# Kernel optimization log

Hardware: AMD Instinct MI355X
Metric: run time of the kernel (lower is better)

The kernel has to match this reference:

```python
import jax, jax.numpy as jnp
import numpy as np

B, W, D, R = 8, 1024, 1024, 64
GAMMA_MIN, GAMMA_MAX, ALPHA_CAP, EPS = 0.15, 1.0, 1.0, 1e-8


def _linear_init(key, fan_in, shape):
    bound = 1.0 / np.sqrt(fan_in)
    return jax.random.uniform(key, shape, jnp.float32, -bound, bound)


def setup_inputs() -> dict:
    key = jax.random.key(0)
    ks = jax.random.split(key, 12)
    h = jax.random.normal(ks[0], (B, W, D), jnp.float32)
    # k_base init as in __init__: exp(-0.15*max(j-i,0)) * tril, row-normalized
    pos = jnp.arange(W, dtype=jnp.float32)
    dist_ji = jnp.clip(pos[None, :] - pos[:, None], 0.0)
    causal = jnp.tril(jnp.ones((W, W), jnp.float32))
    k_init = jnp.exp(-0.15 * dist_ji) * causal
    k_base = k_init / jnp.clip(k_init.sum(axis=1, keepdims=True), 1e-8)
    # decay_logit init: gammas in [0.95, 0.995] -> inverse sigmoid of normalized gamma
    gammas = jnp.linspace(0.95, 0.995, R)
    graw = jnp.clip((gammas - GAMMA_MIN) / (GAMMA_MAX - GAMMA_MIN), 1e-6, 1 - 1e-6)
    decay_logit = jnp.log(graw / (1.0 - graw))
    return {
        "h": h,
        "k_base": k_base,
        "decay_logit": decay_logit,
        "gate_logit": jnp.asarray(8.0, jnp.float32),
        "alpha_logit": jnp.asarray(0.0, jnp.float32),
        "u": 0.05 * jax.random.normal(ks[1], (D, R), jnp.float32),
        "v": 0.05 * jax.random.normal(ks[2], (D, R), jnp.float32),
        "proj_w": _linear_init(ks[3], D, (D, D)),
        "proj_b": _linear_init(ks[4], D, (D,)),
        "norm1_scale": jnp.ones((D,), jnp.float32),
        "norm2_scale": jnp.ones((D,), jnp.float32),
        "up_w": _linear_init(ks[5], D, (2 * D, D)),
        "up_b": _linear_init(ks[6], D, (2 * D,)),
        "down_w": _linear_init(ks[7], 2 * D, (D, 2 * D)),
        "down_b": _linear_init(ks[8], 2 * D, (D,)),
    }


def _rmsnorm(x, scale):
    return x * jax.lax.rsqrt(jnp.mean(x * x, axis=-1, keepdims=True) + 1e-8) * scale


def _l2norm(x):
    # mirrors F.normalize(x, dim=-1, eps=1e-8)
    n = jnp.sqrt(jnp.sum(x * x, axis=-1, keepdims=True))
    return x / jnp.maximum(n, EPS)


def reference(h, k_base, decay_logit, gate_logit, alpha_logit, u, v,
              proj_w, proj_b, norm1_scale, norm2_scale,
              up_w, up_b, down_w, down_b):
    _, w, _ = h.shape
    pos = jnp.arange(w, dtype=h.dtype)
    causal = jnp.tril(jnp.ones((w, w), h.dtype))          # [W, W]
    dist = jnp.clip(pos[:, None] - pos[None, :], 0.0)     # i - j, clamped >= 0

    residual = h
    h_norm = _rmsnorm(h, norm1_scale)

    # dense k_base path (k_base_rank == 0)
    gate = jax.nn.sigmoid(gate_logit)
    kb = k_base[:w, :w] * causal
    out = gate * jnp.einsum('ij,bjd->bid', kb, h_norm)

    # low-rank q/k with per-rank gamma decay (decay_impl='mask')
    qk = h_norm @ jnp.concatenate((u, v), axis=1)          # [B, W, 2R]
    q_raw, k_raw = jnp.split(qk, [u.shape[1]], axis=-1)
    q = _l2norm(q_raw)
    k = _l2norm(k_raw)

    gamma = GAMMA_MIN + (GAMMA_MAX - GAMMA_MIN) * jax.nn.sigmoid(decay_logit)  # [R]
    log_gamma = jnp.log(jnp.clip(gamma, 1e-8))
    decay_mask = jnp.exp(dist[:, :, None] * log_gamma[None, None, :]) * causal[:, :, None]  # [W, W, R]

    alpha = ALPHA_CAP * jax.nn.sigmoid(alpha_logit)
    # scores[b,i,j] = sum_r q[b,i,r] * decay[i,j,r] * k[b,j,r]
    scores = jnp.einsum('bir,ijr,bjr->bij', q, decay_mask, k)
    out = out + alpha * jnp.einsum('bij,bjd->bid', scores, h_norm)

    h1 = residual + (out @ proj_w.T + proj_b)
    # MLP (GELU exact, mult=2), second residual
    m = _rmsnorm(h1, norm2_scale)
    m = jax.nn.gelu(m @ up_w.T + up_b, approximate=False) @ down_w.T + down_b
    return h1 + m
```

## Files before the change

### kernel.cpp

```cpp
#include <hip/hip_runtime.h>
#include <hip/hip_bf16.h>
#include <math.h>

#define B_ 8
#define W_ 1024
#define D_ 1024
#define R_ 64

typedef __hip_bfloat16 bf16;
typedef __attribute__((ext_vector_type(8))) short bf16x8;
typedef __attribute__((ext_vector_type(4))) short short4v;
typedef __attribute__((ext_vector_type(4))) float f32x4;

__device__ __forceinline__ float tof(bf16 x) { return __bfloat162float(x); }
__device__ __forceinline__ short f2bs(float f) {
    bf16 b = __float2bfloat16(f);
    return *(short*)&b;
}

__device__ __forceinline__ void async16(const void* g, void* l) {
    __builtin_amdgcn_global_load_lds(
        (const __attribute__((address_space(1))) unsigned int*)g,
        (__attribute__((address_space(3))) unsigned int*)l,
        16, 0, 0);
}

__device__ __forceinline__ void rmsnorm_body(const float* __restrict__ src,
                                             const float* __restrict__ scale,
                                             bf16* __restrict__ dst, int row,
                                             float* red, float* invs) {
    const float4* x = (const float4*)(src + (size_t)row * D_);
    bf16* y = dst + (size_t)row * D_;
    int t = threadIdx.x;
    float4 v = x[t];
    float ss = v.x * v.x + v.y * v.y + v.z * v.z + v.w * v.w;
#pragma unroll
    for (int off = 32; off; off >>= 1) ss += __shfl_down(ss, off, 64);
    int lane = t & 63, wid = t >> 6;
    if (lane == 0) red[wid] = ss;
    __syncthreads();
    if (t == 0) {
        float s = red[0] + red[1] + red[2] + red[3];
        *invs = rsqrtf(s / (float)D_ + 1e-8f);
    }
    __syncthreads();
    float inv = *invs;
    float4 s4 = ((const float4*)scale)[t];
    short4v o;
    o[0] = f2bs(v.x * inv * s4.x);
    o[1] = f2bs(v.y * inv * s4.y);
    o[2] = f2bs(v.z * inv * s4.z);
    o[3] = f2bs(v.w * inv * s4.w);
    *(short4v*)&y[t * 4] = o;
}

__global__ __launch_bounds__(256)
void rmsnorm_kernel(const float* __restrict__ src, const float* __restrict__ scale,
                    bf16* __restrict__ dst) {
    __shared__ float red[4];
    __shared__ float invs;
    rmsnorm_body(src, scale, dst, blockIdx.x, red, &invs);
}

__global__ __launch_bounds__(256)
void prep_kernel(const float* __restrict__ proj, const float* __restrict__ up,
                 const float* __restrict__ down,
                 bf16* __restrict__ projb, bf16* __restrict__ upb,
                 bf16* __restrict__ downb,
                 const float* __restrict__ u, const float* __restrict__ v,
                 bf16* __restrict__ uvT,
                 const float* __restrict__ h, const float* __restrict__ n1,
                 bf16* __restrict__ hnorm) {
    __shared__ float Ts[64][65];
    __shared__ float red[4];
    __shared__ float invs;
    int bid = blockIdx.x;
    int tid = threadIdx.x;
    if (bid < 2560) {
        size_t idx = ((size_t)bid * 256 + tid) * 8;
        const size_t DD = (size_t)D_ * D_;
        const float* src; bf16* dst; size_t off;
        if (idx < DD)          { src = proj; dst = projb; off = idx; }
        else if (idx < 3 * DD) { src = up;   dst = upb;   off = idx - DD; }
        else                   { src = down; dst = downb; off = idx - 3 * DD; }
        float4 f0 = *(const float4*)(src + off);
        float4 f1 = *(const float4*)(src + off + 4);
        bf16x8 p;
        p[0] = f2bs(f0.x); p[1] = f2bs(f0.y); p[2] = f2bs(f0.z); p[3] = f2bs(f0.w);
        p[4] = f2bs(f1.x); p[5] = f2bs(f1.y); p[6] = f2bs(f1.z); p[7] = f2bs(f1.w);
        *(bf16x8*)(dst + off) = p;
    } else if (bid < 2592) {
        int lb = bid - 2560;
        int g = lb >> 4;
        int d0 = (lb & 15) * 64;
        const float* src = g ? v : u;
#pragma unroll
        for (int e = 0; e < 16; ++e) {
            int idx = tid + e * 256;
            int drow = idx >> 6, rcol = idx & 63;
            Ts[drow][rcol] = src[(size_t)(d0 + drow) * 64 + rcol];
        }
        __syncthreads();
#pragma unroll
        for (int e = 0; e < 16; ++e) {
            int idx = tid + e * 256;
            int orow = idx >> 6, ocol = idx & 63;
            uvT[(size_t)(g * 64 + orow) * D_ + d0 + ocol] = __float2bfloat16(Ts[ocol][orow]);
        }
    } else {
        rmsnorm_body(h, n1, hnorm, bid - 2592, red, &invs);
    }
}

__global__ __launch_bounds__(256)
void transpose_kernel(const bf16* __restrict__ src, bf16* __restrict__ dst) {
    int b = blockIdx.z;
    int j0 = blockIdx.x * 64, d0 = blockIdx.y * 64;
    __shared__ short Ts[64][72];
    const bf16* S = src + (size_t)b * W_ * D_;
    bf16* Dd = dst + (size_t)b * W_ * D_;
    int tid = threadIdx.x;
    int r = tid >> 3, c = (tid & 7) * 8;
#pragma unroll
    for (int p = 0; p < 2; ++p) {
        int j = r + p * 32;
        bf16x8 vv = *(const bf16x8*)&S[(size_t)(j0 + j) * D_ + d0 + c];
#pragma unroll
        for (int e = 0; e < 8; ++e) Ts[j][c + e] = vv[e];
    }
    __syncthreads();
#pragma unroll
    for (int p = 0; p < 2; ++p) {
        int d = r + p * 32;
        bf16x8 vv;
#pragma unroll
        for (int e = 0; e < 8; ++e) vv[e] = Ts[c + e][d];
        *(bf16x8*)&Dd[(size_t)(d0 + d) * W_ + j0 + c] = vv;
    }
}

__global__ __launch_bounds__(128)
void qk_epilogue_kernel(const float* __restrict__ qkraw,
                        const float* __restrict__ decay_logit,
                        float* __restrict__ qg, float* __restrict__ kg) {
    int row = blockIdx.x;
    int i = row & (W_ - 1);
    int t = threadIdx.x;
    int r = t & 63;
    bool isK = t >= 64;
    const size_t PS = (size_t)B_ * W_ * 128;
    size_t off = (size_t)row * 128 + t;
    float val = qkraw[off] + qkraw[PS + off] + qkraw[2 * PS + off] + qkraw[3 * PS + off];
    float sq = val * val;
#pragma unroll
    for (int o = 32; o; o >>= 1) sq += __shfl_xor(sq, o, 64);
    val = val / fmaxf(sqrtf(sq), 1e-8f);

    float dl = decay_logit[r];
    float gamma = 0.15f + 0.85f * (1.f / (1.f + expf(-dl)));
    float lg = logf(gamma);
    float e = isK ? expf(-(float)i * lg) : expf((float)i * lg);
    float o = val * e;
    if (isK) kg[(size_t)row * R_ + r] = o;
    else     qg[(size_t)row * R_ + r] = o;
}

__global__ __launch_bounds__(256)
void buildM_kernel(const float* __restrict__ qg, const float* __restrict__ kg,
                   const float* __restrict__ k_base,
                   const float* __restrict__ gate_logit,
                   const float* __restrict__ alpha_logit,
                   bf16* __restrict__ M) {
    int b = blockIdx.z;
    int ti = blockIdx.y, tj = blockIdx.x;
    if (tj > (ti | 1)) return;
    int i0 = ti * 64, j0 = tj * 64;
    bf16* Mb = M + (size_t)b * W_ * W_;
    int tid = threadIdx.x;

    if (tj > ti) {
        int row = tid >> 2, c0 = (tid & 3) * 16;
        bf16x8 z;
#pragma unroll
        for (int e = 0; e < 8; ++e) z[e] = 0;
        *(bf16x8*)&Mb[(size_t)(i0 + row) * W_ + j0 + c0] = z;
        *(bf16x8*)&Mb[(size_t)(i0 + row) * W_ + j0 + c0 + 8] = z;
        return;
    }

    __shared__ float Qs[64][68];
    __shared__ float Ks[64][68];
#pragma unroll
    for (int e = 0; e < 4; ++e) {
        int idx = tid + e * 256;
        int row = idx >> 4, c4 = (idx & 15) * 4;
        *(float4*)&Qs[row][c4] = *(const float4*)&qg[((size_t)b * W_ + i0 + row) * R_ + c4];
        *(float4*)&Ks[row][c4] = *(const float4*)&kg[((size_t)b * W_ + j0 + row) * R_ + c4];
    }
    __syncthreads();

    int tx = tid & 15, ty = tid >> 4;
    float acc[4][4] = {};
#pragma unroll 4
    for (int rq = 0; rq < 16; ++rq) {
        float4 qa[4], kb[4];
#pragma unroll
        for (int a = 0; a < 4; ++a) qa[a] = *(const float4*)&Qs[ty * 4 + a][rq * 4];
#pragma unroll
        for (int c = 0; c < 4; ++c) kb[c] = *(const float4*)&Ks[tx * 4 + c][rq * 4];
#pragma unroll
        for (int a = 0; a < 4; ++a)
#pragma unroll
            for (int c = 0; c < 4; ++c)
                acc[a][c] += qa[a].x * kb[c].x + qa[a].y * kb[c].y
                           + qa[a].z * kb[c].z + qa[a].w * kb[c].w;
    }

    float gate  = 1.f / (1.f + expf(-(*gate_logit)));
    float alpha = 1.f / (1.f + expf(-(*alpha_logit)));
#pragma unroll
    for (int a = 0; a < 4; ++a) {
        int i = i0 + ty * 4 + a;
        int jb = j0 + tx * 4;
        float4 vkb = *(const float4*)&k_base[(size_t)i * W_ + jb];
        short4v o;
        o[0] = (jb + 0 <= i) ? f2bs(gate * vkb.x + alpha * acc[a][0]) : (short)0;
        o[1] = (jb + 1 <= i) ? f2bs(gate * vkb.y + alpha * acc[a][1]) : (short)0;
        o[2] = (jb + 2 <= i) ? f2bs(gate * vkb.z + alpha * acc[a][2]) : (short)0;
        o[3] = (jb + 3 <= i) ? f2bs(gate * vkb.w + alpha * acc[a][3]) : (short)0;
        *(short4v*)&Mb[(size_t)i * W_ + jb] = o;
    }
}

#define BAR() do { __builtin_amdgcn_sched_barrier(0); \
                   __builtin_amdgcn_s_barrier(); \
                   __builtin_amdgcn_sched_barrier(0); } while (0)

__device__ __forceinline__ void mfma8(const bf16x8 (&fa)[2], const bf16x8 (&fb)[4],
                                      f32x4 (&acc)[2][4]) {
#pragma unroll
    for (int mi = 0; mi < 2; ++mi)
#pragma unroll
        for (int ni = 0; ni < 4; ++ni)
            acc[mi][ni] = __builtin_amdgcn_mfma_f32_16x16x32_bf16(
                fa[mi], fb[ni], acc[mi][ni], 0, 0, 0);
}

__device__ __forceinline__ void readf(const short* At0, const short* Bt0, int slot,
                                      const int (&ao)[2], const int (&bo)[4],
                                      bf16x8 (&fa)[2], bf16x8 (&fb)[4]) {
    const short* Ard = At0 + slot * 4096;
    const short* Brd = Bt0 + slot * 4096;
#pragma unroll
    for (int mi = 0; mi < 2; ++mi) fa[mi] = *(const bf16x8*)&Ard[ao[mi]];
#pragma unroll
    for (int ni = 0; ni < 4; ++ni) fb[ni] = *(const bf16x8*)&Brd[bo[ni]];
}

template<int EPI, int SK>
__global__ __launch_bounds__(512, 4)
void mgemm_kernel(const bf16* __restrict__ A, const bf16* __restrict__ Bm,
                  const float* __restrict__ Res, const float* __restrict__ bias,
                  void* __restrict__ Cout,
                  int M, int N, int K,
                  long sA, long sB, long sC, int causal) {
    __shared__ __align__(16) short At[5][128 * 32];
    __shared__ __align__(16) short Bt[5][128 * 32];
    int z = blockIdx.z;
    const bf16* Ab = (SK > 1) ? A : A + (size_t)z * sA;
    const bf16* Bb = (SK > 1) ? Bm : Bm + (size_t)z * sB;
    int kchunk = K / SK;
    int kbeg = (SK > 1) ? z * kchunk : 0;
    int bx = blockIdx.x;
    if (SK == 1 && causal && z >= (int)(gridDim.z >> 1))
        bx = (int)gridDim.x - 1 - bx;
    int m0 = bx * 128, n0 = blockIdx.y * 128;
    int tid = threadIdx.x;
    int lane = tid & 63, wave = tid >> 6;
    int wy = wave >> 1, wx = wave & 1;
    int quad = lane >> 4, l15 = lane & 15;

    f32x4 acc[2][4];
#pragma unroll
    for (int i = 0; i < 2; ++i)
#pragma unroll
        for (int j = 0; j < 4; ++j)
            acc[i][j] = (f32x4){0.f, 0.f, 0.f, 0.f};

    int kend = kbeg + kchunk;
    if (SK == 1 && causal) kend = (m0 + 128 < K) ? m0 + 128 : K;
    int nIter = (kend - kbeg) >> 5;

    int srcChunk = ((lane & 3) ^ ((lane >> 3) & 3)) * 8;
    size_t rowA = (size_t)(m0 + wave * 16 + (lane >> 2)) * K;
    size_t rowB = (size_t)(n0 + wave * 16 + (lane >> 2)) * K;
    const bf16* aP = Ab + rowA + srcChunk + kbeg;
    const bf16* bP = Bb + rowB + srcChunk + kbeg;
    short* aDst = &At[0][0] + wave * 512;
    short* bDst = &Bt[0][0] + wave * 512;

    int rswz = (quad ^ ((l15 >> 1) & 3)) * 8;
    int ao[2], bo[4];
#pragma unroll
    for (int mi = 0; mi < 2; ++mi) ao[mi] = (wy * 32 + mi * 16 + l15) * 32 + rswz;
#pragma unroll
    for (int ni = 0; ni < 4; ++ni) bo[ni] = (wx * 64 + ni * 16 + l15) * 32 + rswz;

#pragma unroll
    for (int p = 0; p < 4; ++p) {
        async16(aP, aDst + p * 4096);
        async16(bP, bDst + p * 4096);
        aP += 32; bP += 32;
    }
    asm volatile("s_waitcnt vmcnt(6)" ::: "memory");
    BAR();

    bf16x8 fa0[2], fb0[4], fa1[2], fb1[4];
    readf(&At[0][0], &Bt[0][0], 0, ao, bo, fa0, fb0);

    int sStage = 4;
    int sPf = 1;
    int nMain = nIter - 4;

    for (int t = 0; t < nMain; t += 2) {
        asm volatile("s_waitcnt vmcnt(4)" ::: "memory");
        BAR();
        async16(aP, aDst + sStage * 4096);
        async16(bP, bDst + sStage * 4096);
        aP += 32; bP += 32;
        sStage = (sStage == 4) ? 0 : sStage + 1;
        mfma8(fa0, fb0, acc);
        readf(&At[0][0], &Bt[0][0], sPf, ao, bo, fa1, fb1);
        sPf = (sPf == 4) ? 0 : sPf + 1;
        asm volatile("s_waitcnt vmcnt(4)" ::: "memory");
        BAR();
        async16(aP, aDst + sStage * 4096);
        async16(bP, bDst + sStage * 4096);
        aP += 32; bP += 32;
        sStage = (sStage == 4) ? 0 : sStage + 1;
        mfma8(fa1, fb1, acc);
        readf(&At[0][0], &Bt[0][0], sPf, ao, bo, fa0, fb0);
        sPf = (sPf == 4) ? 0 : sPf + 1;
    }

    asm volatile("s_waitcnt vmcnt(4)" ::: "memory");
    BAR();
    mfma8(fa0, fb0, acc);
    readf(&At[0][0], &Bt[0][0], sPf, ao, bo, fa1, fb1);
    sPf = (sPf == 4) ? 0 : sPf + 1;

    asm volatile("s_waitcnt vmcnt(2)" ::: "memory");
    BAR();
    mfma8(fa1, fb1, acc);
    readf(&At[0][0], &Bt[0][0], sPf, ao, bo, fa0, fb0);
    sPf = (sPf == 4) ? 0 : sPf + 1;

    asm volatile("s_waitcnt vmcnt(0)" ::: "memory");
    BAR();
    mfma8(fa0, fb0, acc);
    readf(&At[0][0], &Bt[0][0], sPf, ao, bo, fa1, fb1);

    mfma8(fa1, fb1, acc);

#pragma unroll
    for (int ni = 0; ni < 4; ++ni) {
        int col = n0 + wx * 64 + ni * 16 + l15;
        float bv = (EPI == 1 || EPI == 2) ? bias[col] : 0.f;
#pragma unroll
        for (int mi = 0; mi < 2; ++mi) {
            int row0 = m0 + wy * 32 + mi * 16 + quad * 4;
#pragma unroll
            for (int r = 0; r < 4; ++r) {
                size_t idx = (size_t)(row0 + r) * N + col;
                float val = acc[mi][ni][r];
                if constexpr (EPI == 0) {
                    ((bf16*)Cout)[(size_t)z * sC + idx] = __float2bfloat16(val);
                } else if constexpr (EPI == 1) {
                    ((float*)Cout)[idx] = val + bv + Res[idx];
                } else if constexpr (EPI == 2) {
                    val += bv;
                    val = 0.5f * val * (1.f + erff(val * 0.70710678118654752f));
                    ((bf16*)Cout)[idx] = __float2bfloat16(val);
                } else {
                    ((float*)Cout)[(size_t)z * sC + idx] = val;
                }
            }
        }
    }
}

extern "C" void kernel_launch(void* const* d_in, const int* in_sizes, int n_in,
                              void* d_out, int out_size, void* d_ws, size_t ws_size,
                              hipStream_t stream) {
    const float* h           = (const float*)d_in[0];
    const float* k_base      = (const float*)d_in[1];
    const float* decay_logit = (const float*)d_in[2];
    const float* gate_logit  = (const float*)d_in[3];
    const float* alpha_logit = (const float*)d_in[4];
    const float* u           = (const float*)d_in[5];
    const float* v           = (const float*)d_in[6];
    const float* proj_w      = (const float*)d_in[7];
    const float* proj_b      = (const float*)d_in[8];
    const float* norm1_scale = (const float*)d_in[9];
    const float* norm2_scale = (const float*)d_in[10];
    const float* up_w        = (const float*)d_in[11];
    const float* up_b        = (const float*)d_in[12];
    const float* down_w      = (const float*)d_in[13];
    const float* down_b      = (const float*)d_in[14];

    const size_t MB = 1048576;
    char* ws = (char*)d_ws;
    bf16*  hnorm   = (bf16*)(ws);
    bf16*  uvT     = (bf16*)(ws + 16 * MB);
    float* qg      = (float*)(ws + 16 * MB);
    float* kg      = (float*)(ws + 18 * MB);
    bf16*  hnormT  = (bf16*)(ws + 20 * MB);
    float* qkraw   = (float*)(ws + 36 * MB);
    bf16*  Mbuf    = (bf16*)(ws + 36 * MB);
    bf16*  proj_wb = (bf16*)(ws + 52 * MB);
    bf16*  up_wb   = (bf16*)(ws + 54 * MB);
    bf16*  down_wb = (bf16*)(ws + 58 * MB);
    bf16*  attn    = hnorm;
    bf16*  mnorm   = hnorm;
    bf16*  tbuf    = hnormT;
    float* h1      = (float*)d_out;

    prep_kernel<<<2560 + 32 + B_ * W_, 256, 0, stream>>>(
        proj_w, up_w, down_w, proj_wb, up_wb, down_wb,
        u, v, uvT, h, norm1_scale, hnorm);

    transpose_kernel<<<dim3(W_ / 64, D_ / 64, B_), 256, 0, stream>>>(hnorm, hnormT);

    mgemm_kernel<5, 4><<<dim3(B_ * W_ / 128, 1, 4), 512, 0, stream>>>(
        hnorm, uvT, nullptr, nullptr, qkraw, B_ * W_, 128, D_,
        0, 0, (long)B_ * W_ * 128, 0);

    qk_epilogue_kernel<<<B_ * W_, 128, 0, stream>>>(qkraw, decay_logit, qg, kg);

    buildM_kernel<<<dim3(W_ / 64, W_ / 64, B_), 256, 0, stream>>>(
        qg, kg, k_base, gate_logit, alpha_logit, Mbuf);

    mgemm_kernel<0, 1><<<dim3(W_ / 128, D_ / 128, B_), 512, 0, stream>>>(
        Mbuf, hnormT, nullptr, nullptr, attn, W_, D_, W_,
        (long)W_ * W_, (long)W_ * D_, (long)W_ * D_, 1);

    mgemm_kernel<1, 1><<<dim3(B_ * W_ / 128, D_ / 128, 1), 512, 0, stream>>>(
        attn, proj_wb, h, proj_b, h1, B_ * W_, D_, D_, 0, 0, 0, 0);

    rmsnorm_kernel<<<B_ * W_, 256, 0, stream>>>(h1, norm2_scale, mnorm);

    mgemm_kernel<2, 1><<<dim3(B_ * W_ / 128, 2 * D_ / 128, 1), 512, 0, stream>>>(
        mnorm, up_wb, nullptr, up_b, tbuf, B_ * W_, 2 * D_, D_, 0, 0, 0, 0);

    mgemm_kernel<1, 1><<<dim3(B_ * W_ / 128, D_ / 128, 1), 512, 0, stream>>>(
        tbuf, down_wb, h1, down_b, (float*)d_out, B_ * W_, D_, 2 * D_, 0, 0, 0, 0);
}
```

Before: 330.8 us.

## Restructure GEMM main loop to process two k-steps per barrier

Replaces the deep prologue, steady-state and epilogue software pipeline with a uniform loop. Each iteration waits for all outstanding global-to-LDS loads, issues the loads for the next two k-steps, then reads fragments and runs MFMA for the current two stages. This halves the number of barriers and simplifies control flow. In exchange it cuts prefetch depth and drops fragment-register prefetch, so memory latency may be less well hidden. It also assumes an even number of k-steps.

```diff
diff --git a/kernel.cpp b/kernel.cpp
--- a/kernel.cpp
+++ b/kernel.cpp
@@ -290,6 +290,7 @@
     int kend = kbeg + kchunk;
     if (SK == 1 && causal) kend = (m0 + 128 < K) ? m0 + 128 : K;
     int nIter = (kend - kbeg) >> 5;
+    int P = nIter >> 1;
 
     int srcChunk = ((lane & 3) ^ ((lane >> 3) & 3)) * 8;
     size_t rowA = (size_t)(m0 + wave * 16 + (lane >> 2)) * K;
@@ -306,61 +307,33 @@
 #pragma unroll
     for (int ni = 0; ni < 4; ++ni) bo[ni] = (wx * 64 + ni * 16 + l15) * 32 + rswz;
 
-#pragma unroll
-    for (int p = 0; p < 4; ++p) {
-        async16(aP, aDst + p * 4096);
-        async16(bP, bDst + p * 4096);
-        aP += 32; bP += 32;
-    }
-    asm volatile("s_waitcnt vmcnt(6)" ::: "memory");
-    BAR();
-
+    async16(aP, aDst);          async16(bP, bDst);          aP += 32; bP += 32;
+    async16(aP, aDst + 4096);   async16(bP, bDst + 4096);   aP += 32; bP += 32;
+
+    int sStage = 2;
+    int sCur = 0;
     bf16x8 fa0[2], fb0[4], fa1[2], fb1[4];
-    readf(&At[0][0], &Bt[0][0], 0, ao, bo, fa0, fb0);
-
-    int sStage = 4;
-    int sPf = 1;
-    int nMain = nIter - 4;
-
-    for (int t = 0; t < nMain; t += 2) {
-        asm volatile("s_waitcnt vmcnt(4)" ::: "memory");
+
+    for (int p = 0; p < P; ++p) {
+        asm volatile("s_waitcnt vmcnt(0)" ::: "memory");
         BAR();
-        async16(aP, aDst + sStage * 4096);
-        async16(bP, bDst + sStage * 4096);
-        aP += 32; bP += 32;
-        sStage = (sStage == 4) ? 0 : sStage + 1;
+        if (p + 1 < P) {
+            async16(aP, aDst + sStage * 4096);
+            async16(bP, bDst + sStage * 4096);
+            aP += 32; bP += 32;
+            sStage = (sStage == 4) ? 0 : sStage + 1;
+            async16(aP, aDst + sStage * 4096);
+            async16(bP, bDst + sStage * 4096);
+            aP += 32; bP += 32;
+            sStage = (sStage == 4) ? 0 : sStage + 1;
+        }
+        readf(&At[0][0], &Bt[0][0], sCur, ao, bo, fa0, fb0);
         mfma8(fa0, fb0, acc);
-        readf(&At[0][0], &Bt[0][0], sPf, ao, bo, fa1, fb1);
-        sPf = (sPf == 4) ? 0 : sPf + 1;
-        asm volatile("s_waitcnt vmcnt(4)" ::: "memory");
-        BAR();
-        async16(aP, aDst + sStage * 4096);
-        async16(bP, bDst + sStage * 4096);
-        aP += 32; bP += 32;
-        sStage = (sStage == 4) ? 0 : sStage + 1;
+        sCur = (sCur == 4) ? 0 : sCur + 1;
+        readf(&At[0][0], &Bt[0][0], sCur, ao, bo, fa1, fb1);
         mfma8(fa1, fb1, acc);
-        readf(&At[0][0], &Bt[0][0], sPf, ao, bo, fa0, fb0);
-        sPf = (sPf == 4) ? 0 : sPf + 1;
-    }
-
-    asm volatile("s_waitcnt vmcnt(4)" ::: "memory");
-    BAR();
-    mfma8(fa0, fb0, acc);
-    readf(&At[0][0], &Bt[0][0], sPf, ao, bo, fa1, fb1);
-    sPf = (sPf == 4) ? 0 : sPf + 1;
-
-    asm volatile("s_waitcnt vmcnt(2)" ::: "memory");
-    BAR();
-    mfma8(fa1, fb1, acc);
-    readf(&At[0][0], &Bt[0][0], sPf, ao, bo, fa0, fb0);
-    sPf = (sPf == 4) ? 0 : sPf + 1;
-
-    asm volatile("s_waitcnt vmcnt(0)" ::: "memory");
-    BAR();
-    mfma8(fa0, fb0, acc);
-    readf(&At[0][0], &Bt[0][0], sPf, ao, bo, fa1, fb1);
-
-    mfma8(fa1, fb1, acc);
+        sCur = (sCur == 4) ? 0 : sCur + 1;
+    }
 
 #pragma unroll
     for (int ni = 0; ni < 4; ++ni) {
```

Measured after the change: 333.1 us. Within noise of the previous version (+0.7%).
